# Performance work log

Hardware: AMD Instinct MI355X
Metric: run time of the kernel (lower is better)

The kernel has to match this reference:

```python
import jax, jax.numpy as jnp
import numpy as np

C = 1.5          # Poincare ball curvature (geoopt PoincareBallExact(c=1.5))
TEMP = 0.1       # logits temperature
EPS = 1e-5       # artanh clamp, matches geoopt fp32 eps


def _mlp(x, w1, b1, w2, b2, w3, b3):
    # torch nn.GELU default is the exact erf formulation
    h = jax.nn.gelu(x @ w1 + b1, approximate=False)
    h = jax.nn.gelu(h @ w2 + b2, approximate=False)
    return h @ w3 + b3


def _expmap0(u):
    # geoopt expmap0: tanh(sqrt(c)*||u||) * u / (sqrt(c)*||u||)
    sqrt_c = jnp.sqrt(C)
    n = jnp.maximum(jnp.linalg.norm(u, axis=-1, keepdims=True), 1e-15)
    return jnp.tanh(sqrt_c * n) * u / (sqrt_c * n)


def _poincare_dist(protos, y):
    """Pairwise Poincare distance. protos: (P, d) on-ball, y: (B, d) on-ball -> (B, P).
    dist(x, y) = 2/sqrt(c) * artanh(sqrt(c) * ||mobius_add(-x, y)||)
    """
    sqrt_c = jnp.sqrt(C)
    x = -protos                               # (P, d)
    x2 = jnp.sum(x * x, axis=-1)              # (P,)
    y2 = jnp.sum(y * y, axis=-1)              # (B,)
    xy = y @ x.T                              # (B, P) = <x, y> broadcast
    a = 1.0 + 2.0 * C * xy + C * y2[:, None]  # coeff of x
    b = 1.0 - C * x2[None, :]                 # coeff of y
    denom = 1.0 + 2.0 * C * xy + (C * C) * x2[None, :] * y2[:, None]
    denom = jnp.maximum(jnp.abs(denom), 1e-15)
    # only one (B, P, d) intermediate: the mobius-add numerator
    num = a[:, :, None] * x[None, :, :] + b[:, :, None] * y[:, None, :]
    r = sqrt_c * jnp.linalg.norm(num, axis=-1) / denom   # (B, P)
    r = jnp.clip(r, 0.0, 1.0 - EPS)
    return (2.0 / sqrt_c) * jnp.arctanh(r)


def setup_inputs() -> dict:
    key = jax.random.key(0)
    ks = jax.random.split(key, 16)
    B, DIN, H, D = 64, 768, 4096, 256
    PG, PS = 500, 5000

    def lin(kw, kb, fan_in, fan_out):
        s = 1.0 / np.sqrt(fan_in)
        w = jax.random.uniform(kw, (fan_in, fan_out), jnp.float32, -s, s)
        b = jax.random.uniform(kb, (fan_out,), jnp.float32, -s, s)
        return w, b

    x = jax.random.normal(ks[0], (B, DIN), jnp.float32)
    # prototypes: random points well inside the ball (radius 1/sqrt(1.5) ~ 0.816)
    protos_genus = 0.01 * jax.random.normal(ks[1], (PG, D), jnp.float32)
    protos_species = 0.01 * jax.random.normal(ks[2], (PS, D), jnp.float32)

    w1g, b1g = lin(ks[3], ks[4], DIN, H)
    w2g, b2g = lin(ks[5], ks[6], H, H)
    w3g, b3g = lin(ks[7], ks[8], H, D)
    w1s, b1s = lin(ks[9], ks[10], DIN, H)
    w2s, b2s = lin(ks[11], ks[12], H, H)
    w3s, b3s = lin(ks[13], ks[14], H, D)

    return {
        "x": x, "protos_genus": protos_genus, "protos_species": protos_species,
        "w1g": w1g, "b1g": b1g, "w2g": w2g, "b2g": b2g, "w3g": w3g, "b3g": b3g,
        "w1s": w1s, "b1s": b1s, "w2s": w2s, "b2s": b2s, "w3s": w3s, "b3s": b3s,
    }


def reference(x, protos_genus, protos_species,
              w1g, b1g, w2g, b2g, w3g, b3g,
              w1s, b1s, w2s, b2s, w3s, b3s):
    feat_g = _mlp(x, w1g, b1g, w2g, b2g, w3g, b3g)   # (B, D) euclidean
    feat_s = _mlp(x, w1s, b1s, w2s, b2s, w3s, b3s)
    hyp_g = _expmap0(feat_g)
    hyp_s = _expmap0(feat_s)
    logits_g = -_poincare_dist(protos_genus, hyp_g) / TEMP    # (B, PG)
    logits_s = -_poincare_dist(protos_species, hyp_s) / TEMP  # (B, PS)
    return (logits_g, logits_s)
```

## Files before the change

kernel.cpp:

```cpp
#include <hip/hip_runtime.h>
#include <hip/hip_bf16.h>
#include <math.h>

typedef unsigned short ushort_t;
typedef unsigned int uint_t;

#define C_CURV 1.5f
#define SQRT_C 1.22474487139158905f
#define TEMP_ 0.1f

typedef __attribute__((ext_vector_type(8))) short short8;
typedef __attribute__((ext_vector_type(4))) float f32x4;

static __device__ __forceinline__ ushort_t f2bf(float f) {
  union { float f; uint_t u; } v; v.f = f;
  uint_t u = v.u;
  uint_t r = (u + 0x7FFFu + ((u >> 16) & 1u)) >> 16;
  return (ushort_t)r;
}

static __device__ __forceinline__ float gelu_exact(float x) {
  return 0.5f * x * (1.0f + erff(x * 0.70710678118654752f));
}

#define GLOAD_LDS16(gp, lp) __builtin_amdgcn_global_load_lds( \
    (const __attribute__((address_space(1))) void*)(const void*)(gp), \
    (__attribute__((address_space(3))) void*)(void*)(lp), 16, 0, 0)

__global__ void k_cvt_x(const float* __restrict__ x, ushort_t* __restrict__ xb, int n4) {
  int i = blockIdx.x * blockDim.x + threadIdx.x;
  if (i >= n4) return;
  float4 v = reinterpret_cast<const float4*>(x)[i];
  ushort4 o;
  o.x = f2bf(v.x); o.y = f2bf(v.y); o.z = f2bf(v.z); o.w = f2bf(v.w);
  reinterpret_cast<ushort4*>(xb)[i] = o;
}

__global__ __launch_bounds__(256) void k_gemm(
    const ushort_t* __restrict__ Abase, long a_br_stride,
    const float* __restrict__ Wg, const float* __restrict__ Ws,
    float* __restrict__ partial, int N, int K, int kchunk)
{
  __shared__ float    sW[3][32][256];
  __shared__ ushort_t sA[3][64][32];

  const int tn = blockIdx.x, ks = blockIdx.y, br = blockIdx.z;
  const int KS = gridDim.y;
  const ushort_t* A = Abase + (long)br * a_br_stride;
  const float* W = br ? Ws : Wg;
  const int lane = threadIdx.x & 63;
  const int w = threadIdx.x >> 6;
  const int c = lane & 15;
  const int g = lane >> 4;
  const int n0b = tn * 256;
  const int k0 = ks * kchunk;

  const float* wst = W + (long)(k0 + w * 8) * N + n0b + lane * 4;
  const ushort_t* ast = A + (long)(w * 16 + (lane >> 2)) * K + k0 + (lane & 3) * 8;

  f32x4 acc[4][4];
  #pragma unroll
  for (int mi = 0; mi < 4; ++mi)
    #pragma unroll
    for (int nf = 0; nf < 4; ++nf) acc[mi][nf] = f32x4{0.f, 0.f, 0.f, 0.f};

#define STAGE(buf, t) do { \
    _Pragma("unroll") for (int i = 0; i < 8; ++i) \
      GLOAD_LDS16(wst + (long)((t) * 32 + i) * N, &sW[buf][w * 8 + i][0]); \
    GLOAD_LDS16(ast + (t) * 32, &sA[buf][w * 16][0]); \
  } while (0)

#define COMPUTE(buf) do { \
    short8 af[4]; \
    _Pragma("unroll") for (int mi = 0; mi < 4; ++mi) \
      af[mi] = *reinterpret_cast<const short8*>(&sA[buf][c + 16 * mi][8 * g]); \
    _Pragma("unroll") for (int nf = 0; nf < 4; ++nf) { \
      float bw[8]; \
      _Pragma("unroll") for (int j = 0; j < 8; ++j) \
        bw[j] = sW[buf][8 * g + j][w * 64 + nf * 16 + c]; \
      short8 bf; \
      _Pragma("unroll") for (int j = 0; j < 8; ++j) bf[j] = (short)f2bf(bw[j]); \
      _Pragma("unroll") for (int mi = 0; mi < 4; ++mi) \
        acc[mi][nf] = __builtin_amdgcn_mfma_f32_16x16x32_bf16(af[mi], bf, acc[mi][nf], 0, 0, 0); \
    } \
  } while (0)

  const int nt = kchunk >> 5;
  STAGE(0, 0);
  STAGE(1, 1);
  int t = 0;
  for (; t < nt - 1; ++t) {
    asm volatile("s_waitcnt vmcnt(9)" ::: "memory");
    __builtin_amdgcn_s_barrier();
    if (t + 2 < nt) STAGE((t + 2) % 3, t + 2);
    COMPUTE(t % 3);
  }
  asm volatile("s_waitcnt vmcnt(0)" ::: "memory");
  __builtin_amdgcn_s_barrier();
  COMPUTE(t % 3);
#undef STAGE
#undef COMPUTE

  float* po = partial + (long)(br * KS + ks) * 64 * N;
  #pragma unroll
  for (int mi = 0; mi < 4; ++mi)
    #pragma unroll
    for (int nf = 0; nf < 4; ++nf)
      #pragma unroll
      for (int q = 0; q < 4; ++q) {
        int b = 16 * mi + 4 * g + q;
        po[(long)b * N + n0b + w * 64 + nf * 16 + c] = acc[mi][nf][q];
      }
}

__global__ void k_reduce_gelu(const float* __restrict__ partial,
    const float* __restrict__ bg, const float* __restrict__ bs,
    ushort_t* __restrict__ hb, int N, int KS, int total4)
{
  int i = blockIdx.x * blockDim.x + threadIdx.x;
  if (i >= total4) return;
  int perbr = 64 * N / 4;
  int br = i / perbr;
  int rem = i - br * perbr;
  const float4* pp = reinterpret_cast<const float4*>(partial) + (long)br * KS * perbr + rem;
  float4 s = {0.f, 0.f, 0.f, 0.f};
  #pragma unroll 8
  for (int ks = 0; ks < KS; ++ks) {
    float4 t = pp[(long)ks * perbr];
    s.x += t.x; s.y += t.y; s.z += t.z; s.w += t.w;
  }
  int n4 = rem % (N / 4);
  float4 bv = reinterpret_cast<const float4*>(br ? bs : bg)[n4];
  s.x += bv.x; s.y += bv.y; s.z += bv.z; s.w += bv.w;
  ushort4 o;
  o.x = f2bf(gelu_exact(s.x));
  o.y = f2bf(gelu_exact(s.y));
  o.z = f2bf(gelu_exact(s.z));
  o.w = f2bf(gelu_exact(s.w));
  reinterpret_cast<ushort4*>(hb)[i] = o;
}

__global__ __launch_bounds__(256) void k_expmap(const float* __restrict__ partial,
    const float* __restrict__ b3g, const float* __restrict__ b3s,
    ushort_t* __restrict__ hypb, float* __restrict__ y2, int KS)
{
  int b = blockIdx.x, br = blockIdx.y, d = threadIdx.x;
  const float* pp = partial + (long)(br * KS) * 64 * 256 + (long)b * 256 + d;
  float s = 0.f;
  #pragma unroll 8
  for (int ks = 0; ks < KS; ++ks) s += pp[(long)ks * 64 * 256];
  s += (br ? b3s : b3g)[d];

  float v = s * s;
  #pragma unroll
  for (int off = 1; off < 64; off <<= 1) v += __shfl_xor(v, off);
  __shared__ float red[4];
  __shared__ float n2s;
  if ((threadIdx.x & 63) == 0) red[threadIdx.x >> 6] = v;
  __syncthreads();
  if (threadIdx.x == 0) n2s = red[0] + red[1] + red[2] + red[3];
  __syncthreads();
  float n = fmaxf(sqrtf(n2s), 1e-15f);
  float sn = SQRT_C * n;
  float t = tanhf(sn);
  float scale = t / sn;
  hypb[((long)br * 64 + b) * 256 + d] = f2bf(s * scale);
  if (threadIdx.x == 0) y2[br * 64 + b] = t * t / C_CURV;
}

__global__ __launch_bounds__(256) void k_dist(const float* __restrict__ pg,
    const float* __restrict__ ps, const ushort_t* __restrict__ hypb,
    const float* __restrict__ y2, float* __restrict__ out)
{
  int u = blockIdx.x * 4 + (threadIdx.x >> 6);
  const int lane = threadIdx.x & 63;
  const int c = lane & 15, g = lane >> 4;
  const float* protos; const ushort_t* A; const float* y2p; float* ob; int P;
  if (u < 128) {
    protos = pg; P = 500; A = hypb; y2p = y2; ob = out;
  } else {
    u -= 128;
    if (u >= 1252) return;
    protos = ps; P = 5000; A = hypb + 64 * 256; y2p = y2 + 64; ob = out + 64 * 500;
  }
  const int w = u >> 2;
  const int mi = u & 3;
  int p = w * 16 + c;
  int pc = min(p, P - 1);
  const float* pp = protos + (long)pc * 256 + 8 * g;
  const ushort_t* ap = A + (long)(c + 16 * mi) * 256 + 8 * g;

  f32x4 acc = {0.f, 0.f, 0.f, 0.f};
  float x2p = 0.f;

  #pragma unroll
  for (int s8 = 0; s8 < 8; ++s8) {
    float4 v0 = *reinterpret_cast<const float4*>(pp + 32 * s8);
    float4 v1 = *reinterpret_cast<const float4*>(pp + 32 * s8 + 4);
    x2p += v0.x * v0.x + v0.y * v0.y + v0.z * v0.z + v0.w * v0.w
         + v1.x * v1.x + v1.y * v1.y + v1.z * v1.z + v1.w * v1.w;
    short8 bfr;
    bfr[0] = (short)f2bf(v0.x); bfr[1] = (short)f2bf(v0.y);
    bfr[2] = (short)f2bf(v0.z); bfr[3] = (short)f2bf(v0.w);
    bfr[4] = (short)f2bf(v1.x); bfr[5] = (short)f2bf(v1.y);
    bfr[6] = (short)f2bf(v1.z); bfr[7] = (short)f2bf(v1.w);
    short8 af = *reinterpret_cast<const short8*>(ap + 32 * s8);
    acc = __builtin_amdgcn_mfma_f32_16x16x32_bf16(af, bfr, acc, 0, 0, 0);
  }
  x2p += __shfl_xor(x2p, 16);
  x2p += __shfl_xor(x2p, 32);
  const float x2 = x2p;
  const float bb = 1.f - C_CURV * x2;
  const float LC = -2.f / (SQRT_C * TEMP_);

  if (p < P) {
    #pragma unroll
    for (int q = 0; q < 4; ++q) {
      int b = 16 * mi + 4 * g + q;
      float xy = -acc[q];
      float y2v = y2p[b];
      float a = 1.f + 2.f * C_CURV * xy + C_CURV * y2v;
      float den = fabsf(1.f + 2.f * C_CURV * xy + C_CURV * C_CURV * x2 * y2v);
      den = fmaxf(den, 1e-15f);
      float num2 = a * a * x2 + 2.f * a * bb * xy + bb * bb * y2v;
      num2 = fmaxf(num2, 0.f);
      float r = SQRT_C * sqrtf(num2) / den;
      r = fminf(r, 1.f - 1e-5f);
      r = fmaxf(r, 0.f);
      ob[(long)b * P + p] = LC * atanhf(r);
    }
  }
}

extern "C" void kernel_launch(void* const* d_in, const int* in_sizes, int n_in,
                              void* d_out, int out_size, void* d_ws, size_t ws_size,
                              hipStream_t stream) {
  const float* x   = (const float*)d_in[0];
  const float* pg  = (const float*)d_in[1];
  const float* ps  = (const float*)d_in[2];
  const float* w1g = (const float*)d_in[3];
  const float* b1g = (const float*)d_in[4];
  const float* w2g = (const float*)d_in[5];
  const float* b2g = (const float*)d_in[6];
  const float* w3g = (const float*)d_in[7];
  const float* b3g = (const float*)d_in[8];
  const float* w1s = (const float*)d_in[9];
  const float* b1s = (const float*)d_in[10];
  const float* w2s = (const float*)d_in[11];
  const float* b2s = (const float*)d_in[12];
  const float* w3s = (const float*)d_in[13];
  const float* b3s = (const float*)d_in[14];
  float* out = (float*)d_out;
  char* ws = (char*)d_ws;
  (void)in_sizes; (void)n_in; (void)out_size; (void)ws_size;

  const int KS1 = 6, KS2 = 8, KS3 = 64;
  size_t PART = (size_t)KS2 * 2 * 64 * 4096 * 4;

  float*    partial = (float*)   (ws);
  ushort_t* xb      = (ushort_t*)(ws + PART);
  ushort_t* h1b     = (ushort_t*)(ws + PART + 98304);
  ushort_t* h2b     = (ushort_t*)(ws + PART + 98304 + 1048576);
  ushort_t* hypb    = (ushort_t*)(ws + PART + 98304 + 2097152);
  float*    y2      = (float*)   (ws + PART + 98304 + 2097152 + 65536);

  k_cvt_x<<<48, 256, 0, stream>>>(x, xb, 64 * 768 / 4);
  k_gemm<<<dim3(16, KS1, 2), 256, 0, stream>>>(xb, 0L, w1g, w1s, partial, 4096, 768, 768 / KS1);
  k_reduce_gelu<<<512, 256, 0, stream>>>(partial, b1g, b1s, h1b, 4096, KS1, 2 * 64 * 4096 / 4);
  k_gemm<<<dim3(16, KS2, 2), 256, 0, stream>>>(h1b, (long)64 * 4096, w2g, w2s, partial, 4096, 4096, 4096 / KS2);
  k_reduce_gelu<<<512, 256, 0, stream>>>(partial, b2g, b2s, h2b, 4096, KS2, 2 * 64 * 4096 / 4);
  k_gemm<<<dim3(1, KS3, 2), 256, 0, stream>>>(h2b, (long)64 * 4096, w3g, w3s, partial, 256, 4096, 4096 / KS3);
  k_expmap<<<dim3(64, 2), 256, 0, stream>>>(partial, b3g, b3s, hypb, y2, KS3);
  k_dist<<<345, 256, 0, stream>>>(pg, ps, hypb, y2, out);
}
```

Measured before the change: 84.32 us.

## Store split-K partials in bf16 and deepen GEMM pipeline to four stages

Split-K partial sums are now written and read as bf16 rather than fp32, which halves partial-buffer traffic between the GEMM and the reduce/expmap kernels. The reduce kernel is widened to handle 8 elements per thread. The GEMM LDS ring grows from 3 to 4 stages with a deeper prefetch, and the third layer uses half as many K splits. Rounding partials to bf16 before summing costs accuracy, and the larger LDS footprint may lower occupancy.

```diff
diff --git a/kernel.cpp b/kernel.cpp
--- a/kernel.cpp
+++ b/kernel.cpp
@@ -17,6 +17,11 @@
   uint_t u = v.u;
   uint_t r = (u + 0x7FFFu + ((u >> 16) & 1u)) >> 16;
   return (ushort_t)r;
+}
+
+static __device__ __forceinline__ float b2f(ushort_t h) {
+  union { uint_t u; float f; } v; v.u = ((uint_t)h) << 16;
+  return v.f;
 }
 
 static __device__ __forceinline__ float gelu_exact(float x) {
@@ -39,10 +44,10 @@
 __global__ __launch_bounds__(256) void k_gemm(
     const ushort_t* __restrict__ Abase, long a_br_stride,
     const float* __restrict__ Wg, const float* __restrict__ Ws,
-    float* __restrict__ partial, int N, int K, int kchunk)
-{
-  __shared__ float    sW[3][32][256];
-  __shared__ ushort_t sA[3][64][32];
+    ushort_t* __restrict__ partial, int N, int K, int kchunk)
+{
+  __shared__ float    sW[4][32][256];
+  __shared__ ushort_t sA[4][64][32];
 
   const int tn = blockIdx.x, ks = blockIdx.y, br = blockIdx.z;
   const int KS = gridDim.y;
@@ -88,20 +93,27 @@
   const int nt = kchunk >> 5;
   STAGE(0, 0);
   STAGE(1, 1);
+  STAGE(2, 2);
   int t = 0;
-  for (; t < nt - 1; ++t) {
-    asm volatile("s_waitcnt vmcnt(9)" ::: "memory");
+  for (; t + 3 < nt; ++t) {
+    asm volatile("s_waitcnt vmcnt(18)" ::: "memory");
     __builtin_amdgcn_s_barrier();
-    if (t + 2 < nt) STAGE((t + 2) % 3, t + 2);
-    COMPUTE(t % 3);
-  }
+    STAGE((t + 3) & 3, t + 3);
+    COMPUTE(t & 3);
+  }
+  asm volatile("s_waitcnt vmcnt(18)" ::: "memory");
+  __builtin_amdgcn_s_barrier();
+  COMPUTE(t & 3); ++t;
+  asm volatile("s_waitcnt vmcnt(9)" ::: "memory");
+  __builtin_amdgcn_s_barrier();
+  COMPUTE(t & 3); ++t;
   asm volatile("s_waitcnt vmcnt(0)" ::: "memory");
   __builtin_amdgcn_s_barrier();
-  COMPUTE(t % 3);
+  COMPUTE(t & 3);
 #undef STAGE
 #undef COMPUTE
 
-  float* po = partial + (long)(br * KS + ks) * 64 * N;
+  ushort_t* po = partial + (long)(br * KS + ks) * 64 * N;
   #pragma unroll
   for (int mi = 0; mi < 4; ++mi)
     #pragma unroll
@@ -109,46 +121,46 @@
       #pragma unroll
       for (int q = 0; q < 4; ++q) {
         int b = 16 * mi + 4 * g + q;
-        po[(long)b * N + n0b + w * 64 + nf * 16 + c] = acc[mi][nf][q];
+        po[(long)b * N + n0b + w * 64 + nf * 16 + c] = f2bf(acc[mi][nf][q]);
       }
 }
 
-__global__ void k_reduce_gelu(const float* __restrict__ partial,
+__global__ void k_reduce_gelu(const ushort_t* __restrict__ partial,
     const float* __restrict__ bg, const float* __restrict__ bs,
-    ushort_t* __restrict__ hb, int N, int KS, int total4)
+    ushort_t* __restrict__ hb, int N, int KS, int total8)
 {
   int i = blockIdx.x * blockDim.x + threadIdx.x;
-  if (i >= total4) return;
-  int perbr = 64 * N / 4;
-  int br = i / perbr;
-  int rem = i - br * perbr;
-  const float4* pp = reinterpret_cast<const float4*>(partial) + (long)br * KS * perbr + rem;
-  float4 s = {0.f, 0.f, 0.f, 0.f};
-  #pragma unroll 8
+  if (i >= total8) return;
+  int perbr8 = 64 * N / 8;
+  int br = i / perbr8;
+  int rem = i - br * perbr8;
+  const short8* pp = reinterpret_cast<const short8*>(partial) + (long)br * KS * perbr8 + rem;
+  float s[8] = {0.f, 0.f, 0.f, 0.f, 0.f, 0.f, 0.f, 0.f};
   for (int ks = 0; ks < KS; ++ks) {
-    float4 t = pp[(long)ks * perbr];
-    s.x += t.x; s.y += t.y; s.z += t.z; s.w += t.w;
-  }
-  int n4 = rem % (N / 4);
-  float4 bv = reinterpret_cast<const float4*>(br ? bs : bg)[n4];
-  s.x += bv.x; s.y += bv.y; s.z += bv.z; s.w += bv.w;
-  ushort4 o;
-  o.x = f2bf(gelu_exact(s.x));
-  o.y = f2bf(gelu_exact(s.y));
-  o.z = f2bf(gelu_exact(s.z));
-  o.w = f2bf(gelu_exact(s.w));
-  reinterpret_cast<ushort4*>(hb)[i] = o;
-}
-
-__global__ __launch_bounds__(256) void k_expmap(const float* __restrict__ partial,
+    short8 t = pp[(long)ks * perbr8];
+    #pragma unroll
+    for (int j = 0; j < 8; ++j) s[j] += b2f((ushort_t)t[j]);
+  }
+  int n8 = rem % (N / 8);
+  float4 bv0 = reinterpret_cast<const float4*>(br ? bs : bg)[n8 * 2];
+  float4 bv1 = reinterpret_cast<const float4*>(br ? bs : bg)[n8 * 2 + 1];
+  s[0] += bv0.x; s[1] += bv0.y; s[2] += bv0.z; s[3] += bv0.w;
+  s[4] += bv1.x; s[5] += bv1.y; s[6] += bv1.z; s[7] += bv1.w;
+  short8 o;
+  #pragma unroll
+  for (int j = 0; j < 8; ++j) o[j] = (short)f2bf(gelu_exact(s[j]));
+  reinterpret_cast<short8*>(hb)[i] = o;
+}
+
+__global__ __launch_bounds__(256) void k_expmap(const ushort_t* __restrict__ partial,
     const float* __restrict__ b3g, const float* __restrict__ b3s,
     ushort_t* __restrict__ hypb, float* __restrict__ y2, int KS)
 {
   int b = blockIdx.x, br = blockIdx.y, d = threadIdx.x;
-  const float* pp = partial + (long)(br * KS) * 64 * 256 + (long)b * 256 + d;
+  const ushort_t* pp = partial + (long)(br * KS) * 64 * 256 + (long)b * 256 + d;
   float s = 0.f;
   #pragma unroll 8
-  for (int ks = 0; ks < KS; ++ks) s += pp[(long)ks * 64 * 256];
+  for (int ks = 0; ks < KS; ++ks) s += b2f(pp[(long)ks * 64 * 256]);
   s += (br ? b3s : b3g)[d];
 
   float v = s * s;
@@ -254,10 +266,10 @@
   char* ws = (char*)d_ws;
   (void)in_sizes; (void)n_in; (void)out_size; (void)ws_size;
 
-  const int KS1 = 6, KS2 = 8, KS3 = 64;
-  size_t PART = (size_t)KS2 * 2 * 64 * 4096 * 4;
-
-  float*    partial = (float*)   (ws);
+  const int KS1 = 6, KS2 = 8, KS3 = 32;
+  size_t PART = (size_t)KS2 * 2 * 64 * 4096 * 2;
+
+  ushort_t* partial = (ushort_t*)(ws);
   ushort_t* xb      = (ushort_t*)(ws + PART);
   ushort_t* h1b     = (ushort_t*)(ws + PART + 98304);
   ushort_t* h2b     = (ushort_t*)(ws + PART + 98304 + 1048576);
@@ -266,9 +278,9 @@
 
   k_cvt_x<<<48, 256, 0, stream>>>(x, xb, 64 * 768 / 4);
   k_gemm<<<dim3(16, KS1, 2), 256, 0, stream>>>(xb, 0L, w1g, w1s, partial, 4096, 768, 768 / KS1);
-  k_reduce_gelu<<<512, 256, 0, stream>>>(partial, b1g, b1s, h1b, 4096, KS1, 2 * 64 * 4096 / 4);
+  k_reduce_gelu<<<256, 256, 0, stream>>>(partial, b1g, b1s, h1b, 4096, KS1, 2 * 64 * 4096 / 8);
   k_gemm<<<dim3(16, KS2, 2), 256, 0, stream>>>(h1b, (long)64 * 4096, w2g, w2s, partial, 4096, 4096, 4096 / KS2);
-  k_reduce_gelu<<<512, 256, 0, stream>>>(partial, b2g, b2s, h2b, 4096, KS2, 2 * 64 * 4096 / 4);
+  k_reduce_gelu<<<256, 256, 0, stream>>>(partial, b2g, b2s, h2b, 4096, KS2, 2 * 64 * 4096 / 8);
   k_gemm<<<dim3(1, KS3, 2), 256, 0, stream>>>(h2b, (long)64 * 4096, w3g, w3s, partial, 256, 4096, 4096 / KS3);
   k_expmap<<<dim3(64, 2), 256, 0, stream>>>(partial, b3g, b3s, hypb, y2, KS3);
   k_dist<<<345, 256, 0, stream>>>(pg, ps, hypb, y2, out);
```

Measured after the change: 85.09 us. No clear change (+0.9%).
